# Kernel optimization log

Hardware: AMD Instinct MI355X
Metric: run time of the kernel (lower is better)

## Reference

```python
import jax, jax.numpy as jnp
import numpy as np

K_UPPER = 196608  # number of smallest-|grad| positions to mask per sample


def setup_inputs() -> dict:
    key = jax.random.key(0)
    k1, k2 = jax.random.split(key)
    x = jax.random.normal(k1, (64, 3, 512, 512), dtype=jnp.float32)
    grad = jax.random.normal(k2, (64, 3, 512, 512), dtype=jnp.float32)
    return {"x": x, "grad": grad}


def _mask_low_gradient(x, grad):
    # x, grad: [B, C, H, W]
    B, C, H, W = x.shape
    hw = H * W
    flat_g = grad.reshape(B, -1)                                  # [B, C*H*W]
    # _sort: k smallest absolute gradients -> top_k of negated abs (unsorted ok)
    _neg_vals, idx = jax.lax.top_k(-jnp.abs(flat_g), K_UPPER)     # idx: [B, K]
    # channel containing each selected flat index (matches the torch range test)
    ch = idx // hw                                                # [B, K]
    xc = x.reshape(B, C, hw)
    # Faithful to source: torch slice [start:channel_indexes] EXCLUDES the last
    # element of each channel when computing min/max.
    mn = jnp.min(xc[:, :, : hw - 1], axis=-1)                     # [B, C]
    mx = jnp.max(xc[:, :, : hw - 1], axis=-1)                     # [B, C]
    lo = jnp.take_along_axis(mn, ch, axis=1)                      # [B, K]
    hi = jnp.take_along_axis(mx, ch, axis=1)                      # [B, K]
    # uniform fill in [lo, hi) per masked element
    u = jax.random.uniform(jax.random.key(42), idx.shape, dtype=x.dtype)
    fill = lo + u * (hi - lo)                                     # [B, K]
    flat_x = x.reshape(B, -1)
    out = flat_x.at[jnp.arange(B)[:, None], idx].set(fill)
    return out.reshape(x.shape)


def reference(x, grad):
    return _mask_low_gradient(x, grad)
```

## Files before the change

kernel.cpp:

```cpp
#include <hip/hip_runtime.h>
#include <stdint.h>

#define TPB 256
#define TPS 1024

constexpr int BN   = 64;
constexpr int CCH  = 3;
constexpr int HWS  = 262144;
constexpr int LOG_HW = 18;
constexpr int NPS  = 786432;
constexpr int KSEL = 196608;
constexpr int KCAP = 200704;
constexpr int NB_T = 32;
constexpr int CH_T = NPS / NB_T;
constexpr int NB_C = 64;
constexpr int CH_C = NPS / NB_C;
constexpr int WCH  = CH_C / 4;
constexpr int NB_S = 8;
constexpr int CH_S = KCAP / NB_S;
constexpr int TILE = 4096;
constexpr int NBINS = 2048;
constexpr int SUB  = 8;
constexpr int NFB  = 49;
constexpr int ASLOT = 1024;
constexpr int ACAP = 256 * ASLOT;

typedef unsigned u32x4 __attribute__((ext_vector_type(4)));

constexpr int WS_MN   = 0;
constexpr int WS_MX   = 192;
constexpr int WS_V1   = 384;
constexpr int WS_B1   = 448;
constexpr int WS_V2   = 512;
constexpr int WS_GS   = 576;
constexpr int WS_KP   = 640;
constexpr int WS_S0   = 704;
constexpr int WS_S01  = 768;
constexpr int WS_CNT  = 832;
constexpr int WS_COFF = WS_CNT + BN * 256;
constexpr int WS_MNP  = WS_COFF + BN * 256;
constexpr int WS_MXP  = WS_MNP + BN * CCH * SUB;
constexpr int WS_CNT2 = WS_MXP + BN * CCH * SUB;
constexpr int WS_RC   = WS_CNT2 + BN * 256;
constexpr int WS_CHC  = WS_RC + BN * 256;
constexpr int WS_THA  = WS_CHC + BN * 4;
constexpr int WS_THB  = WS_THA + BN * NBINS;
constexpr int WS_H0   = WS_THB + BN * NBINS;
constexpr int WS_H1   = WS_H0 + BN * 256 * NB_S;
constexpr int WS_H2   = WS_H1 + BN * 256 * NB_S;
constexpr int WS_H3   = WS_H2 + BN * 256 * NB_S;
constexpr int WS_HF   = WS_H3 + BN * 256 * NB_S;
constexpr size_t WS_FIX_END = (size_t)WS_HF + (size_t)BN * 64 * NB_S;
constexpr size_t RECW = (size_t)BN * KCAP * 2;
constexpr size_t WS_NEEDED_BYTES = (WS_FIX_END + 2 * RECW) * 4;
static_assert((size_t)BN * ACAP <= RECW, "append scratch must fit in R2");

__device__ __forceinline__ unsigned rotl32(unsigned x, int r) { return (x << r) | (x >> (32 - r)); }

__device__ __forceinline__ void tf4(unsigned& x0, unsigned& x1, int a, int b, int c, int d) {
  x0 += x1; x1 = rotl32(x1, a); x1 ^= x0;
  x0 += x1; x1 = rotl32(x1, b); x1 ^= x0;
  x0 += x1; x1 = rotl32(x1, c); x1 ^= x0;
  x0 += x1; x1 = rotl32(x1, d); x1 ^= x0;
}

__device__ __forceinline__ void threefry2x32(unsigned k0, unsigned k1, unsigned c0, unsigned c1,
                                             unsigned& o0, unsigned& o1) {
  const unsigned ks2 = k0 ^ k1 ^ 0x1BD11BDAu;
  unsigned x0 = c0 + k0, x1 = c1 + k1;
  tf4(x0, x1, 13, 15, 26, 6);  x0 += k1;  x1 += ks2 + 1u;
  tf4(x0, x1, 17, 29, 16, 24); x0 += ks2; x1 += k0 + 2u;
  tf4(x0, x1, 13, 15, 26, 6);  x0 += k0;  x1 += k1 + 3u;
  tf4(x0, x1, 17, 29, 16, 24); x0 += k1;  x1 += ks2 + 4u;
  tf4(x0, x1, 13, 15, 26, 6);  x0 += ks2; x1 += k0 + 5u;
  o0 = x0; o1 = x1;
}

__global__ __launch_bounds__(TPB) void k_zero(unsigned* __restrict__ p, int n) {
  int i = blockIdx.x * TPB + threadIdx.x;
  if (i < n) p[i] = 0u;
}

__global__ __launch_bounds__(TPB) void k_mnmx(const float4* __restrict__ x,
                                              unsigned* __restrict__ ws) {
  __shared__ float smn[TPB], smx[TPB];
  const int g = blockIdx.x;
  const int bc = g / SUB, sub = g - bc * SUB;
  const int Q4 = HWS / 4 / SUB;
  const size_t base4 = (size_t)bc * (HWS / 4) + (size_t)sub * Q4;
  const bool last = (sub == SUB - 1);
  const int tid = threadIdx.x;
  float lo = 3.4e38f, hi = -3.4e38f;
  for (int i = tid; i < Q4; i += TPB) {
    float4 v = x[base4 + i];
    if (last && i == Q4 - 1) {
      lo = fminf(lo, fminf(fminf(v.x, v.y), v.z));
      hi = fmaxf(hi, fmaxf(fmaxf(v.x, v.y), v.z));
    } else {
      lo = fminf(lo, fminf(fminf(v.x, v.y), fminf(v.z, v.w)));
      hi = fmaxf(hi, fmaxf(fmaxf(v.x, v.y), fmaxf(v.z, v.w)));
    }
  }
  smn[tid] = lo; smx[tid] = hi; __syncthreads();
  for (int s = TPB / 2; s > 0; s >>= 1) {
    if (tid < s) { smn[tid] = fminf(smn[tid], smn[tid + s]); smx[tid] = fmaxf(smx[tid], smx[tid + s]); }
    __syncthreads();
  }
  if (tid == 0) {
    ((float*)(ws + WS_MNP))[g] = smn[0];
    ((float*)(ws + WS_MXP))[g] = smx[0];
  }
}

__global__ __launch_bounds__(TPB) void k_mnfin(unsigned* __restrict__ ws) {
  const int t = threadIdx.x;
  if (t < BN * CCH) {
    const float* mnp = (const float*)(ws + WS_MNP);
    const float* mxp = (const float*)(ws + WS_MXP);
    float lo = 3.4e38f, hi = -3.4e38f;
    for (int s = 0; s < SUB; ++s) {
      lo = fminf(lo, mnp[t * SUB + s]);
      hi = fmaxf(hi, mxp[t * SUB + s]);
    }
    ((float*)(ws + WS_MN))[t] = lo;
    ((float*)(ws + WS_MX))[t] = hi;
  }
}

__global__ __launch_bounds__(TPB) void k_thrA(const unsigned* __restrict__ gb, unsigned* __restrict__ hist) {
  __shared__ unsigned h[NBINS];
  const int b = blockIdx.y, blk = blockIdx.x, tid = threadIdx.x;
  for (int v = tid; v < NBINS; v += TPB) h[v] = 0u;
  __syncthreads();
  const uint4* g4 = (const uint4*)(gb + (size_t)b * NPS + (size_t)blk * CH_T);
  for (int i = tid; i < CH_T / 4; i += TPB) {
    uint4 v = g4[i];
    atomicAdd(&h[(v.x & 0x7FFFFFFFu) >> 21], 1u);
    atomicAdd(&h[(v.y & 0x7FFFFFFFu) >> 21], 1u);
    atomicAdd(&h[(v.z & 0x7FFFFFFFu) >> 21], 1u);
    atomicAdd(&h[(v.w & 0x7FFFFFFFu) >> 21], 1u);
  }
  __syncthreads();
  unsigned* gh = hist + (size_t)b * NBINS;
  for (int v = tid; v < NBINS; v += TPB) if (h[v]) atomicAdd(&gh[v], h[v]);
}

__global__ __launch_bounds__(TPB) void k_thrBC(const unsigned* __restrict__ gb,
                                               unsigned* __restrict__ hist,
                                               unsigned* __restrict__ app,
                                               unsigned* __restrict__ ws) {
  __shared__ unsigned h[NBINS];
  __shared__ unsigned chs[3];
  const int bid = blockIdx.x;
  const int b = bid & 63, blk = bid >> 6, tid = threadIdx.x;
  const int lane = tid & 63, wv = tid >> 6;
  const unsigned long long ltm = (1ull << lane) - 1ull;
  for (int v = tid; v < NBINS; v += TPB) h[v] = 0u;
  if (tid < 3) chs[tid] = 0u;
  __syncthreads();
  const unsigned V1 = ws[WS_V1 + b];
  const unsigned rangeId = (unsigned)(blk * 4 + wv);
  const uint4* g4 = (const uint4*)(gb + (size_t)b * NPS + (size_t)blk * CH_C) + wv * (WCH / 4);
  const unsigned e0 = (unsigned)blk * CH_C + (unsigned)wv * WCH;
  unsigned* ap = app + (size_t)b * ACAP + (size_t)rangeId * ASLOT;
  unsigned abase = 0;
  unsigned cntLess = 0, cc0 = 0, cc1 = 0, cc2 = 0;
  for (int it = 0; it < WCH / 256; ++it) {
    const uint4 v = g4[it * 64 + lane];
    const unsigned e = e0 + (unsigned)it * 256u + (unsigned)lane * 4u;
    const unsigned k[4] = { v.x & 0x7FFFFFFFu, v.y & 0x7FFFFFFFu, v.z & 0x7FFFFFFFu, v.w & 0x7FFFFFFFu };
#pragma unroll
    for (int c = 0; c < 4; ++c) {
      const unsigned top = k[c] >> 21;
      const bool isEq = (top == V1);
      if (top < V1) {
        ++cntLess;
        const unsigned ch = (e + (unsigned)c) >> LOG_HW;
        if (ch == 0) ++cc0; else if (ch == 1) ++cc1; else ++cc2;
      } else if (isEq) {
        atomicAdd(&h[(k[c] >> 10) & 2047u], 1u);
      }
      unsigned long long m = __ballot(isEq);
      if (isEq) {
        const unsigned ai = abase + (unsigned)__popcll(m & ltm);
        if (ai < (unsigned)ASLOT) {
          const unsigned ch = (e + (unsigned)c) >> LOG_HW;
          ap[ai] = (ch << 11) | ((k[c] >> 10) & 2047u);
        }
      }
      abase += (unsigned)__popcll(m);
    }
  }
  if (lane == 0) ws[WS_RC + b * 256 + rangeId] = min(abase, (unsigned)ASLOT);
  for (int off = 32; off >= 1; off >>= 1) cntLess += __shfl_down(cntLess, off, 64);
  if (lane == 0) ws[WS_CNT + b * 256 + rangeId] = cntLess;
  if (cc0) atomicAdd(&chs[0], cc0);
  if (cc1) atomicAdd(&chs[1], cc1);
  if (cc2) atomicAdd(&chs[2], cc2);
  __syncthreads();
  if (tid < 3 && chs[tid]) atomicAdd(&ws[WS_CHC + b * 4 + tid], chs[tid]);
  unsigned* gh = hist + (size_t)b * NBINS;
  for (int v = tid; v < NBINS; v += TPB) if (h[v]) atomicAdd(&gh[v], h[v]);
}

__global__ __launch_bounds__(TPB) void k_find(const unsigned* __restrict__ hist,
                                              unsigned* __restrict__ ws, int mode) {
  __shared__ unsigned part[TPB];
  const int b = blockIdx.x, tid = threadIdx.x;
  const unsigned* h = hist + (size_t)b * NBINS;
  const int per = NBINS / TPB;
  const unsigned Kt = (mode == 0) ? (unsigned)KSEL : (unsigned)KSEL - ws[WS_B1 + b];
  unsigned vals[8];
  unsigned s = 0;
  for (int j = 0; j < per; ++j) { vals[j] = h[tid * per + j]; s += vals[j]; }
  part[tid] = s; __syncthreads();
  for (int off = 1; off < TPB; off <<= 1) {
    unsigned t = (tid >= off) ? part[tid - off] : 0u;
    __syncthreads(); part[tid] += t; __syncthreads();
  }
  unsigned run = part[tid] - s;
  for (int j = 0; j < per; ++j) {
    const unsigned lo = run, c = vals[j];
    run += c;
    if (lo < Kt && Kt <= run) {
      const unsigned v = (unsigned)(tid * per + j);
      if (mode == 0) {
        ws[WS_V1 + b] = v; ws[WS_B1 + b] = lo;
      } else {
        ws[WS_V2 + b] = v;
        const unsigned T22 = (ws[WS_V1 + b] << 11) | v;
        ws[WS_GS + b] = (T22 << 10) | 1023u;
        unsigned kp = ws[WS_B1 + b] + lo + c;
        if (kp > (unsigned)KCAP) kp = (unsigned)KCAP;
        ws[WS_KP + b] = kp;
      }
    }
  }
}

__global__ __launch_bounds__(TPB) void k_cc2(const unsigned* __restrict__ app,
                                             unsigned* __restrict__ ws) {
  __shared__ unsigned lch[3];
  const int b = blockIdx.x, tid = threadIdx.x;
  if (tid < 3) lch[tid] = 0u;
  __syncthreads();
  const unsigned V2 = ws[WS_V2 + b];
  const unsigned cnt = ws[WS_RC + b * 256 + tid];
  const unsigned* ap = app + (size_t)b * ACAP + (size_t)tid * ASLOT;
  unsigned n2 = 0, c0 = 0, c1 = 0, c2 = 0;
  for (unsigned i = 0; i < cnt; ++i) {
    const unsigned e = ap[i];
    if ((e & 2047u) <= V2) {
      ++n2;
      const unsigned ch = (e >> 11) & 3u;
      if (ch == 0) ++c0; else if (ch == 1) ++c1; else ++c2;
    }
  }
  ws[WS_CNT2 + b * 256 + tid] = n2;
  if (c0) atomicAdd(&lch[0], c0);
  if (c1) atomicAdd(&lch[1], c1);
  if (c2) atomicAdd(&lch[2], c2);
  __syncthreads();
  if (tid < 3 && lch[tid]) atomicAdd(&ws[WS_CHC + b * 4 + tid], lch[tid]);
}

__global__ __launch_bounds__(TPB) void k_cscan(unsigned* __restrict__ ws) {
  __shared__ unsigned wsum[4];
  const int b = blockIdx.x, tid = threadIdx.x;
  const int lane = tid & 63, wv = tid >> 6;
  const unsigned cnt = ws[WS_CNT + b * 256 + tid] + ws[WS_CNT2 + b * 256 + tid];
  unsigned incl = cnt;
  for (int off = 1; off < 64; off <<= 1) {
    unsigned t = __shfl_up(incl, off, 64);
    if (lane >= off) incl += t;
  }
  if (lane == 63) wsum[wv] = incl;
  __syncthreads();
  unsigned wpre = 0;
  for (int w = 0; w < wv; ++w) wpre += wsum[w];
  ws[WS_COFF + b * 256 + tid] = incl - cnt + wpre;
  if (tid == 0) {
    const unsigned s0 = ws[WS_CHC + b * 4 + 0];
    ws[WS_S0 + b] = s0;
    ws[WS_S01 + b] = s0 + ws[WS_CHC + b * 4 + 1];
  }
}

__global__ __launch_bounds__(TPB) void k_cscatter(const unsigned* __restrict__ gb,
                                                  const unsigned* __restrict__ ws,
                                                  unsigned* __restrict__ keyArr,
                                                  unsigned* __restrict__ H0) {
  __shared__ unsigned h2[256 * NB_S];
  const int bid = blockIdx.x;
  const int b = bid & 63, blk = bid >> 6, tid = threadIdx.x;
  const int lane = tid & 63, wv = tid >> 6;
  for (int e = tid; e < 256 * NB_S; e += TPB) h2[e] = 0u;
  __syncthreads();
  const unsigned G = ws[WS_GS + b];
  unsigned base = ws[WS_COFF + b * 256 + blk * 4 + wv];
  const uint4* g4 = (const uint4*)(gb + (size_t)b * NPS + (size_t)blk * CH_C) + wv * (WCH / 4);
  unsigned* ka = keyArr + (size_t)b * KCAP;
  for (int it = 0; it < WCH / 256; ++it) {
    const uint4 v = g4[it * 64 + lane];
    unsigned k[4] = { v.x & 0x7FFFFFFFu, v.y & 0x7FFFFFFFu, v.z & 0x7FFFFFFFu, v.w & 0x7FFFFFFFu };
    bool s[4];
    unsigned cnt = 0;
#pragma unroll
    for (int c = 0; c < 4; ++c) { s[c] = (k[c] <= G); cnt += (unsigned)s[c]; }
    unsigned incl = cnt;
    for (int off = 1; off < 64; off <<= 1) {
      unsigned u = __shfl_up(incl, off, 64);
      if (lane >= off) incl += u;
    }
    const unsigned wtot = __shfl(incl, 63, 64);
    unsigned pos = base + incl - cnt;
#pragma unroll
    for (int c = 0; c < 4; ++c) {
      if (s[c]) {
        if (pos < (unsigned)KCAP) {
          ka[pos] = k[c];
          atomicAdd(&h2[(k[c] & 255u) * NB_S + pos / (unsigned)CH_S], 1u);
        }
        ++pos;
      }
    }
    base += wtot;
  }
  __syncthreads();
  unsigned* Hb = H0 + (size_t)b * 256 * NB_S;
  for (int e = tid; e < 256 * NB_S; e += TPB) {
    unsigned c = h2[e];
    if (c) atomicAdd(&Hb[e], c);
  }
}

__global__ __launch_bounds__(TPB) void k_hscan(unsigned* __restrict__ H) {
  __shared__ unsigned wsum[4];
  const int b = blockIdx.x, tid = threadIdx.x;
  const int lane = tid & 63, wv = tid >> 6;
  unsigned* Hb = H + (size_t)b * 256 * NB_S;
  unsigned row[NB_S];
  unsigned run = 0;
#pragma unroll
  for (int k = 0; k < NB_S; ++k) {
    unsigned t = Hb[tid * NB_S + k];
    row[k] = run; run += t;
  }
  unsigned incl = run;
  for (int off = 1; off < 64; off <<= 1) {
    unsigned t = __shfl_up(incl, off, 64);
    if (lane >= off) incl += t;
  }
  if (lane == 63) wsum[wv] = incl;
  __syncthreads();
  unsigned wpre = 0;
  for (int w = 0; w < wv; ++w) wpre += wsum[w];
  const unsigned excl = incl - run + wpre;
#pragma unroll
  for (int k = 0; k < NB_S; ++k) Hb[tid * NB_S + k] = row[k] + excl;
}

__global__ __launch_bounds__(64) void k_hscanF(unsigned* __restrict__ Hf) {
  const int b = blockIdx.x, tid = threadIdx.x;
  unsigned* Hb = Hf + (size_t)b * 64 * NB_S;
  unsigned row[NB_S];
  unsigned run = 0;
  if (tid < NFB) {
#pragma unroll
    for (int k = 0; k < NB_S; ++k) {
      unsigned t = Hb[tid * NB_S + k];
      row[k] = run; run += t;
    }
  }
  unsigned incl = run;
  for (int off = 1; off < 64; off <<= 1) {
    unsigned t = __shfl_up(incl, off, 64);
    if (tid >= off) incl += t;
  }
  const unsigned excl = incl - run;
  if (tid < NFB) {
#pragma unroll
    for (int k = 0; k < NB_S; ++k) Hb[tid * NB_S + k] = row[k] + excl;
  }
}

template<int MODE>
__global__ __launch_bounds__(TPS) void k_sort8(const unsigned* __restrict__ keyIn,
                                               const uint2* __restrict__ inR,
                                               uint2* __restrict__ outR,
                                               const unsigned* __restrict__ Hcur,
                                               unsigned* __restrict__ Hnext,
                                               unsigned* __restrict__ Hf,
                                               const unsigned* __restrict__ ws,
                                               int shift) {
  __shared__ unsigned wh[16][256];
  __shared__ unsigned gout[256];
  __shared__ unsigned gbase[256];
  __shared__ unsigned wsum[4];
  __shared__ uint2    stg[TILE];
  __shared__ unsigned h2[256 * NB_S];
  __shared__ unsigned h2f[(MODE == 1) ? NFB * NB_S : 1];
  const int bid = blockIdx.x;
  const int b = bid & 63, blk = bid >> 6, tid = threadIdx.x;
  const int lane = tid & 63, wv = tid >> 6;
  const unsigned long long ltm = (1ull << lane) - 1ull;
  const unsigned kp = min(ws[WS_KP + b], (unsigned)KCAP);
  const unsigned s0 = (unsigned)blk * CH_S;
  const unsigned s1 = min(s0 + (unsigned)CH_S, kp);
  const unsigned* ki = keyIn + (size_t)b * KCAP;
  const uint2* in = inR + (size_t)b * KCAP;
  uint2* out = outR + (size_t)b * KCAP;
  const bool doF = (MODE == 1) && (Hf != nullptr);

  for (int d = tid; d < 256; d += TPS) gbase[d] = Hcur[((size_t)b * 256 + d) * NB_S + blk];
  for (int e = tid; e < 256 * NB_S; e += TPS) h2[e] = 0u;
  if (MODE == 1) { if (doF) for (int e = tid; e < NFB * NB_S; e += TPS) h2f[e] = 0u; }
  __syncthreads();

  for (unsigned t0 = s0; t0 < s1; t0 += (unsigned)TILE) {
    { uint4* w4 = (uint4*)&wh[0][0];
      w4[tid] = make_uint4(0u, 0u, 0u, 0u); }
    __syncthreads();

    unsigned key[4], cpp[4], wloc[4], dig[4];
    bool val[4];
    const unsigned wbase = t0 + (unsigned)wv * 256u;
#pragma unroll
    for (int c = 0; c < 4; ++c) {
      const unsigned i = wbase + (unsigned)c * 64u + (unsigned)lane;
      val[c] = (i < s1);
      if (MODE == 0) { cpp[c] = i; key[c] = val[c] ? ki[i] : 0u; }
      else { uint2 r = val[c] ? in[i] : make_uint2(0u, 0u); cpp[c] = r.x; key[c] = r.y; }
      dig[c] = (key[c] >> shift) & 255u;
      unsigned long long peers = __ballot(val[c]);
#pragma unroll
      for (int bit = 0; bit < 8; ++bit) {
        unsigned long long bb = __ballot(val[c] && ((dig[c] >> bit) & 1u));
        peers &= ((dig[c] >> bit) & 1u) ? bb : ~bb;
      }
      const unsigned before = (unsigned)__popcll(peers & ltm);
      int ldr = __ffsll((unsigned long long)peers) - 1;
      if (ldr < 0) ldr = 0;
      unsigned old = 0;
      if (val[c] && lane == ldr) old = atomicAdd(&wh[wv][dig[c]], (unsigned)__popcll(peers));
      old = __shfl(old, ldr, 64);
      wloc[c] = old + before;
    }
    __syncthreads();

    unsigned incl = 0, tot = 0;
    if (tid < 256) {
      const unsigned d = (unsigned)tid;
#pragma unroll
      for (int w = 0; w < 16; ++w) tot += wh[w][d];
      incl = tot;
      for (int off = 1; off < 64; off <<= 1) {
        unsigned t = __shfl_up(incl, off, 64);
        if (lane >= off) incl += t;
      }
      if (lane == 63) wsum[wv] = incl;
    }
    __syncthreads();
    if (tid < 256) {
      const unsigned d = (unsigned)tid;
      unsigned wpre = 0;
      for (int w = 0; w < wv; ++w) wpre += wsum[w];
      const unsigned tstart = incl - tot + wpre;
      const unsigned g = gbase[d];
      gout[d] = g - tstart;
      gbase[d] = g + tot;
      unsigned run = tstart;
#pragma unroll
      for (int w = 0; w < 16; ++w) { const unsigned t = wh[w][d]; wh[w][d] = run; run += t; }
    }
    __syncthreads();

#pragma unroll
    for (int c = 0; c < 4; ++c) {
      if (val[c]) {
        uint2 r; r.x = cpp[c]; r.y = key[c];
        stg[wh[wv][dig[c]] + wloc[c]] = r;
      }
    }
    __syncthreads();
    const unsigned nt = min((unsigned)TILE, s1 - t0);
    for (unsigned j = tid; j < nt; j += TPS) {
      const uint2 r = stg[j];
      const unsigned d = (r.y >> shift) & 255u;
      const unsigned pos = gout[d] + j;
      out[pos] = r;
      const unsigned nd = (r.y >> (shift + 8)) & 255u;
      atomicAdd(&h2[nd * NB_S + pos / (unsigned)CH_S], 1u);
      if (doF) atomicAdd(&h2f[(r.x >> 12) * NB_S + pos / (unsigned)CH_S], 1u);
    }
    __syncthreads();
  }

  {
    unsigned* Hb = Hnext + (size_t)b * 256 * NB_S;
    for (int e = tid; e < 256 * NB_S; e += TPS) {
      unsigned c = h2[e];
      if (c) atomicAdd(&Hb[e], c);
    }
    if (doF) {
      unsigned* Hfb = Hf + (size_t)b * 64 * NB_S;
      for (int e = tid; e < NFB * NB_S; e += TPS) {
        unsigned c = h2f[e];
        if (c) atomicAdd(&Hfb[e], c);
      }
    }
  }
}

__global__ __launch_bounds__(TPS) void k_final(const uint2* __restrict__ inR,
                                               uint2* __restrict__ pairOut,
                                               const unsigned* __restrict__ Hcur,
                                               const unsigned* __restrict__ Hf,
                                               const unsigned* __restrict__ ws) {
  __shared__ unsigned wh[16][128];
  __shared__ unsigned gbase[128];
  __shared__ unsigned whF[16][64];
  __shared__ unsigned goutF[64];
  __shared__ unsigned gbaseF[64];
  __shared__ uint2    stg[TILE];
  const int bid = blockIdx.x;
  const int b = bid & 63, blk = bid >> 6, tid = threadIdx.x;
  const int lane = tid & 63, wv = tid >> 6;
  const unsigned long long ltm = (1ull << lane) - 1ull;
  const unsigned kp = min(ws[WS_KP + b], (unsigned)KCAP);
  const unsigned s0 = (unsigned)blk * CH_S;
  const unsigned s1 = min(s0 + (unsigned)CH_S, kp);
  const uint2* in = inR + (size_t)b * KCAP;
  uint2* po = pairOut + (size_t)b * KCAP;

  for (int d = tid; d < 128; d += TPS) gbase[d] = Hcur[((size_t)b * 256 + d) * NB_S + blk];
  for (int d = tid; d < 64; d += TPS)
    gbaseF[d] = (d < NFB) ? Hf[((size_t)b * 64 + d) * NB_S + blk] : 0u;
  __syncthreads();

  for (unsigned t0 = s0; t0 < s1; t0 += (unsigned)TILE) {
    { uint4* p = (uint4*)&wh[0][0];
      if (tid < 512) p[tid] = make_uint4(0u, 0u, 0u, 0u);
      uint4* q = (uint4*)&whF[0][0];
      if (tid >= 512 && tid < 768) q[tid - 512] = make_uint4(0u, 0u, 0u, 0u); }
    __syncthreads();

    unsigned key[4], cpp[4], wloc[4], dig[4];
    bool val[4];
    const unsigned wbase = t0 + (unsigned)wv * 256u;
#pragma unroll
    for (int c = 0; c < 4; ++c) {
      const unsigned i = wbase + (unsigned)c * 64u + (unsigned)lane;
      val[c] = (i < s1);
      uint2 r = val[c] ? in[i] : make_uint2(0u, 0u);
      cpp[c] = r.x; key[c] = r.y;
      dig[c] = (key[c] >> 24) & 127u;
      unsigned long long peers = __ballot(val[c]);
#pragma unroll
      for (int bit = 0; bit < 7; ++bit) {
        unsigned long long bb = __ballot(val[c] && ((dig[c] >> bit) & 1u));
        peers &= ((dig[c] >> bit) & 1u) ? bb : ~bb;
      }
      const unsigned before = (unsigned)__popcll(peers & ltm);
      int ldr = __ffsll((unsigned long long)peers) - 1;
      if (ldr < 0) ldr = 0;
      unsigned old = 0;
      if (val[c] && lane == ldr) old = atomicAdd(&wh[wv][dig[c]], (unsigned)__popcll(peers));
      old = __shfl(old, ldr, 64);
      wloc[c] = old + before;
    }
    __syncthreads();

    if (tid < 128) {
      const unsigned d = (unsigned)tid;
      unsigned run = gbase[d];
#pragma unroll
      for (int w = 0; w < 16; ++w) { const unsigned t = wh[w][d]; wh[w][d] = run; run += t; }
      gbase[d] = run;
    }
    __syncthreads();

    unsigned rnk[4], dbF[4], wlocF[4];
#pragma unroll
    for (int c = 0; c < 4; ++c) {
      dbF[c] = cpp[c] >> 12;
      if (val[c]) {
        rnk[c] = wh[wv][dig[c]] + wloc[c];
        wlocF[c] = atomicAdd(&whF[wv][dbF[c]], 1u);
      }
    }
    __syncthreads();

    if (tid < 64) {
      const unsigned d = (unsigned)tid;
      unsigned tot = 0;
      if (d < NFB) {
#pragma unroll
        for (int w = 0; w < 16; ++w) tot += whF[w][d];
      }
      unsigned incl = tot;
      for (int off = 1; off < 64; off <<= 1) {
        unsigned t = __shfl_up(incl, off, 64);
        if (lane >= off) incl += t;
      }
      const unsigned tstart = incl - tot;
      goutF[d] = gbaseF[d] - tstart;
      gbaseF[d] += tot;
      unsigned run = tstart;
#pragma unroll
      for (int w = 0; w < 16; ++w) { const unsigned t = whF[w][d]; whF[w][d] = run; run += t; }
    }
    __syncthreads();

#pragma unroll
    for (int c = 0; c < 4; ++c) {
      if (val[c]) {
        uint2 r; r.x = cpp[c]; r.y = rnk[c];
        stg[whF[wv][dbF[c]] + wlocF[c]] = r;
      }
    }
    __syncthreads();

    const unsigned nt = min((unsigned)TILE, s1 - t0);
    for (unsigned j = tid; j < nt; j += TPS) {
      const uint2 r = stg[j];
      po[goutF[r.x >> 12] + j] = r;
    }
    __syncthreads();
  }
}

__global__ __launch_bounds__(TPB) void k_unpack(const uint2* __restrict__ pairs,
                                                unsigned* __restrict__ fm,
                                                const unsigned* __restrict__ ws) {
  __shared__ unsigned vals[4096];
  const int bid = blockIdx.x;
  const int b = bid & 63, d = bid >> 6, tid = threadIdx.x;
  const unsigned kp = min(ws[WS_KP + b], (unsigned)KCAP);
  const unsigned start = (unsigned)d * 4096u;
  if (start >= kp) return;
  const unsigned cnt = min(4096u, kp - start);
  const unsigned S0 = ws[WS_S0 + b], S01 = ws[WS_S01 + b];
  const float* mnf = (const float*)(ws + WS_MN);
  const float* mxf = (const float*)(ws + WS_MX);
  const float l0 = mnf[b * CCH], l1 = mnf[b * CCH + 1], l2 = mnf[b * CCH + 2];
  const float h0 = mxf[b * CCH], h1 = mxf[b * CCH + 1], h2v = mxf[b * CCH + 2];
  const uint2* pb = pairs + (size_t)b * KCAP + start;
  for (unsigned j = tid; j < cnt; j += TPB) {
    const uint2 r = pb[j];
    unsigned res = 0xFFFFFFFFu;
    if (r.y < (unsigned)KSEL) {
      const unsigned p = (unsigned)b * (unsigned)KSEL + r.y;
      unsigned o0, o1;
      threefry2x32(0u, 42u, 0u, p, o0, o1);
      const unsigned bits = o0 ^ o1;
      const float u = __uint_as_float((bits >> 9) | 0x3f800000u) - 1.0f;
      const unsigned ch = (unsigned)(r.x >= S0) + (unsigned)(r.x >= S01);
      const float lo = (ch == 0) ? l0 : ((ch == 1) ? l1 : l2);
      const float hi = (ch == 0) ? h0 : ((ch == 1) ? h1 : h2v);
      res = __float_as_uint(lo + u * (hi - lo));
    }
    vals[r.x & 4095u] = res;
  }
  __syncthreads();
  unsigned* f = fm + (size_t)b * KCAP + start;
  for (unsigned j = tid; j < cnt; j += TPB) f[j] = vals[j];
}

__global__ __launch_bounds__(TPB) void k_fill(const u32x4* __restrict__ x4,
                                              const u32x4* __restrict__ g4all,
                                              const unsigned* __restrict__ fillmap,
                                              const unsigned* __restrict__ ws,
                                              u32x4* __restrict__ out4) {
  const int bid = blockIdx.x;
  const int b = bid & 63, blk = bid >> 6, tid = threadIdx.x;
  const int lane = tid & 63, wv = tid >> 6;
  const unsigned G = ws[WS_GS + b];
  const unsigned kp = min(ws[WS_KP + b], (unsigned)KCAP);
  unsigned base = ws[WS_COFF + b * 256 + blk * 4 + wv];
  const size_t t4 = (size_t)b * (NPS / 4) + (size_t)blk * (CH_C / 4) + (size_t)wv * (WCH / 4);
  const unsigned* fm = fillmap + (size_t)b * KCAP;
  for (int it = 0; it < WCH / 256; ++it) {
    const size_t a = t4 + it * 64 + lane;
    const u32x4 gv = __builtin_nontemporal_load(&g4all[a]);
    u32x4 xv = __builtin_nontemporal_load(&x4[a]);
    unsigned k[4] = { gv.x & 0x7FFFFFFFu, gv.y & 0x7FFFFFFFu, gv.z & 0x7FFFFFFFu, gv.w & 0x7FFFFFFFu };
    bool s[4];
    unsigned cnt = 0;
#pragma unroll
    for (int c = 0; c < 4; ++c) { s[c] = (k[c] <= G); cnt += (unsigned)s[c]; }
    unsigned incl = cnt;
    for (int off = 1; off < 64; off <<= 1) {
      unsigned u = __shfl_up(incl, off, 64);
      if (lane >= off) incl += u;
    }
    const unsigned wtot = __shfl(incl, 63, 64);
    unsigned pos = base + incl - cnt;
#pragma unroll
    for (int c = 0; c < 4; ++c) {
      if (s[c]) {
        if (pos < kp) {
          const unsigned r = fm[pos];
          if (r != 0xFFFFFFFFu) xv[c] = r;
        }
        ++pos;
      }
    }
    __builtin_nontemporal_store(xv, &out4[a]);
    base += wtot;
  }
}

extern "C" void kernel_launch(void* const* d_in, const int* in_sizes, int n_in,
                              void* d_out, int out_size, void* d_ws, size_t ws_size,
                              hipStream_t stream) {
  const float* x = (const float*)d_in[0];
  const unsigned* gb = (const unsigned*)d_in[1];
  float* out = (float*)d_out;
  unsigned* ws = (unsigned*)d_ws;
  if (ws_size < WS_NEEDED_BYTES) return;

  unsigned* R1 = ws + WS_FIX_END;
  unsigned* R2 = ws + WS_FIX_END + RECW;
  unsigned* H0 = ws + WS_H0;
  unsigned* H1 = ws + WS_H1;
  unsigned* H2 = ws + WS_H2;
  unsigned* H3 = ws + WS_H3;
  unsigned* HF = ws + WS_HF;

  dim3 blk(TPB);
  dim3 sblk(TPS);

  k_mnmx<<<dim3(BN * CCH * SUB), blk, 0, stream>>>((const float4*)x, ws);
  k_mnfin<<<dim3(1), blk, 0, stream>>>(ws);
  {
    const int nz = (int)(WS_FIX_END - WS_CHC);
    k_zero<<<dim3((nz + TPB - 1) / TPB), blk, 0, stream>>>(ws + WS_CHC, nz);
  }

  k_thrA<<<dim3(NB_T, BN), blk, 0, stream>>>(gb, ws + WS_THA);
  k_find<<<dim3(BN), blk, 0, stream>>>(ws + WS_THA, ws, 0);
  k_thrBC<<<dim3(NB_C * BN), blk, 0, stream>>>(gb, ws + WS_THB, R2, ws);
  k_find<<<dim3(BN), blk, 0, stream>>>(ws + WS_THB, ws, 1);
  k_cc2<<<dim3(BN), blk, 0, stream>>>(R2, ws);
  k_cscan<<<dim3(BN), blk, 0, stream>>>(ws);

  k_cscatter<<<dim3(NB_C * BN), blk, 0, stream>>>(gb, ws, R1, H0);

  k_hscan<<<dim3(BN), blk, 0, stream>>>(H0);
  k_sort8<0><<<dim3(NB_S * BN), sblk, 0, stream>>>(R1, (const uint2*)nullptr, (uint2*)R2, H0, H1, nullptr, ws, 0);
  k_hscan<<<dim3(BN), blk, 0, stream>>>(H1);
  k_sort8<1><<<dim3(NB_S * BN), sblk, 0, stream>>>(nullptr, (const uint2*)R2, (uint2*)R1, H1, H2, nullptr, ws, 8);
  k_hscan<<<dim3(BN), blk, 0, stream>>>(H2);
  k_sort8<1><<<dim3(NB_S * BN), sblk, 0, stream>>>(nullptr, (const uint2*)R1, (uint2*)R2, H2, H3, HF, ws, 16);
  k_hscan<<<dim3(BN), blk, 0, stream>>>(H3);
  k_hscanF<<<dim3(BN), dim3(64), 0, stream>>>(HF);

  k_final<<<dim3(NB_S * BN), sblk, 0, stream>>>((const uint2*)R2, (uint2*)R1, H3, HF, ws);
  k_unpack<<<dim3(NFB * BN), blk, 0, stream>>>((const uint2*)R1, R2, ws);

  k_fill<<<dim3(NB_C * BN), blk, 0, stream>>>((const u32x4*)x, (const u32x4*)gb, R2, ws, (u32x4*)out);
}
```

Baseline: 707.0 us.

## Write selection bitmap in scatter pass and read it in fill instead of grad

The compaction scatter kernel now packs the per-element selection predicate (|g| <= G) into a bitmap, one bit per element. The fill kernel reads this bitmap instead of re-reading the full gradient tensor, which cuts a large stream of global memory reads from the final pass. Ranges were also split three ways (768 per sample instead of 256) with smaller append slots, and the counting, scan and cc2 kernels were adapted to match. The bitmap path is used only when the workspace is large enough, otherwise the old path runs. The cost is extra bitmap writes and some shuffles in the scatter kernel.

```diff
diff --git a/kernel.cpp b/kernel.cpp
--- a/kernel.cpp
+++ b/kernel.cpp
@@ -15,15 +15,16 @@
 constexpr int CH_T = NPS / NB_T;
 constexpr int NB_C = 64;
 constexpr int CH_C = NPS / NB_C;
-constexpr int WCH  = CH_C / 4;
+constexpr int NRNG = 768;
 constexpr int NB_S = 8;
 constexpr int CH_S = KCAP / NB_S;
 constexpr int TILE = 4096;
 constexpr int NBINS = 2048;
 constexpr int SUB  = 8;
 constexpr int NFB  = 49;
-constexpr int ASLOT = 1024;
-constexpr int ACAP = 256 * ASLOT;
+constexpr int ASLOT = 256;
+constexpr int ACAP = NRNG * ASLOT;
+constexpr int BMPW = NPS / 32;
 
 typedef unsigned u32x4 __attribute__((ext_vector_type(4)));
 
@@ -37,12 +38,12 @@
 constexpr int WS_S0   = 704;
 constexpr int WS_S01  = 768;
 constexpr int WS_CNT  = 832;
-constexpr int WS_COFF = WS_CNT + BN * 256;
-constexpr int WS_MNP  = WS_COFF + BN * 256;
+constexpr int WS_COFF = WS_CNT + BN * NRNG;
+constexpr int WS_MNP  = WS_COFF + BN * NRNG;
 constexpr int WS_MXP  = WS_MNP + BN * CCH * SUB;
 constexpr int WS_CNT2 = WS_MXP + BN * CCH * SUB;
-constexpr int WS_RC   = WS_CNT2 + BN * 256;
-constexpr int WS_CHC  = WS_RC + BN * 256;
+constexpr int WS_RC   = WS_CNT2 + BN * NRNG;
+constexpr int WS_CHC  = WS_RC + BN * NRNG;
 constexpr int WS_THA  = WS_CHC + BN * 4;
 constexpr int WS_THB  = WS_THA + BN * NBINS;
 constexpr int WS_H0   = WS_THB + BN * NBINS;
@@ -53,6 +54,8 @@
 constexpr size_t WS_FIX_END = (size_t)WS_HF + (size_t)BN * 64 * NB_S;
 constexpr size_t RECW = (size_t)BN * KCAP * 2;
 constexpr size_t WS_NEEDED_BYTES = (WS_FIX_END + 2 * RECW) * 4;
+constexpr size_t WS_BMP_OFF = WS_FIX_END + 2 * RECW;
+constexpr size_t WS_NEEDED_BMP = (WS_BMP_OFF + (size_t)BN * BMPW) * 4;
 static_assert((size_t)BN * ACAP <= RECW, "append scratch must fit in R2");
 
 __device__ __forceinline__ unsigned rotl32(unsigned x, int r) { return (x << r) | (x >> (32 - r)); }
@@ -159,41 +162,47 @@
   if (tid < 3) chs[tid] = 0u;
   __syncthreads();
   const unsigned V1 = ws[WS_V1 + b];
-  const unsigned rangeId = (unsigned)(blk * 4 + wv);
-  const uint4* g4 = (const uint4*)(gb + (size_t)b * NPS + (size_t)blk * CH_C) + wv * (WCH / 4);
-  const unsigned e0 = (unsigned)blk * CH_C + (unsigned)wv * WCH;
-  unsigned* ap = app + (size_t)b * ACAP + (size_t)rangeId * ASLOT;
-  unsigned abase = 0;
-  unsigned cntLess = 0, cc0 = 0, cc1 = 0, cc2 = 0;
-  for (int it = 0; it < WCH / 256; ++it) {
-    const uint4 v = g4[it * 64 + lane];
-    const unsigned e = e0 + (unsigned)it * 256u + (unsigned)lane * 4u;
-    const unsigned k[4] = { v.x & 0x7FFFFFFFu, v.y & 0x7FFFFFFFu, v.z & 0x7FFFFFFFu, v.w & 0x7FFFFFFFu };
-#pragma unroll
-    for (int c = 0; c < 4; ++c) {
-      const unsigned top = k[c] >> 21;
-      const bool isEq = (top == V1);
-      if (top < V1) {
-        ++cntLess;
-        const unsigned ch = (e + (unsigned)c) >> LOG_HW;
-        if (ch == 0) ++cc0; else if (ch == 1) ++cc1; else ++cc2;
-      } else if (isEq) {
-        atomicAdd(&h[(k[c] >> 10) & 2047u], 1u);
-      }
-      unsigned long long m = __ballot(isEq);
-      if (isEq) {
-        const unsigned ai = abase + (unsigned)__popcll(m & ltm);
-        if (ai < (unsigned)ASLOT) {
+  const uint4* g4 = (const uint4*)(gb + (size_t)b * NPS + (size_t)blk * CH_C) + wv * 768;
+  unsigned cc0 = 0, cc1 = 0, cc2 = 0;
+  for (int r = 0; r < 3; ++r) {
+    const unsigned rangeId = (unsigned)((blk * 4 + wv) * 3 + r);
+    unsigned* ap = app + (size_t)b * ACAP + (size_t)rangeId * ASLOT;
+    unsigned abase = 0, cntLess = 0;
+#pragma unroll
+    for (int it = 0; it < 4; ++it) {
+      const uint4 v = g4[r * 256 + it * 64 + lane];
+      const unsigned e = (unsigned)blk * CH_C + (unsigned)wv * 3072u + (unsigned)r * 1024u
+                       + (unsigned)it * 256u + (unsigned)lane * 4u;
+      const unsigned k[4] = { v.x & 0x7FFFFFFFu, v.y & 0x7FFFFFFFu, v.z & 0x7FFFFFFFu, v.w & 0x7FFFFFFFu };
+#pragma unroll
+      for (int c = 0; c < 4; ++c) {
+        const unsigned top = k[c] >> 21;
+        const bool isEq = (top == V1);
+        if (top < V1) {
+          ++cntLess;
           const unsigned ch = (e + (unsigned)c) >> LOG_HW;
-          ap[ai] = (ch << 11) | ((k[c] >> 10) & 2047u);
+          if (ch == 0) ++cc0; else if (ch == 1) ++cc1; else ++cc2;
+        } else if (isEq) {
+          atomicAdd(&h[(k[c] >> 10) & 2047u], 1u);
         }
-      }
-      abase += (unsigned)__popcll(m);
-    }
-  }
-  if (lane == 0) ws[WS_RC + b * 256 + rangeId] = min(abase, (unsigned)ASLOT);
-  for (int off = 32; off >= 1; off >>= 1) cntLess += __shfl_down(cntLess, off, 64);
-  if (lane == 0) ws[WS_CNT + b * 256 + rangeId] = cntLess;
+        unsigned long long m = __ballot(isEq);
+        if (isEq) {
+          const unsigned ai = abase + (unsigned)__popcll(m & ltm);
+          if (ai < (unsigned)ASLOT) {
+            const unsigned ch = (e + (unsigned)c) >> LOG_HW;
+            ap[ai] = (ch << 11) | ((k[c] >> 10) & 2047u);
+          }
+        }
+        abase += (unsigned)__popcll(m);
+      }
+    }
+    unsigned cl = cntLess;
+    for (int off = 32; off >= 1; off >>= 1) cl += __shfl_down(cl, off, 64);
+    if (lane == 0) {
+      ws[WS_CNT + b * NRNG + rangeId] = cl;
+      ws[WS_RC + b * NRNG + rangeId] = min(abase, (unsigned)ASLOT);
+    }
+  }
   if (cc0) atomicAdd(&chs[0], cc0);
   if (cc1) atomicAdd(&chs[1], cc1);
   if (cc2) atomicAdd(&chs[2], cc2);
@@ -245,18 +254,22 @@
   if (tid < 3) lch[tid] = 0u;
   __syncthreads();
   const unsigned V2 = ws[WS_V2 + b];
-  const unsigned cnt = ws[WS_RC + b * 256 + tid];
-  const unsigned* ap = app + (size_t)b * ACAP + (size_t)tid * ASLOT;
-  unsigned n2 = 0, c0 = 0, c1 = 0, c2 = 0;
-  for (unsigned i = 0; i < cnt; ++i) {
-    const unsigned e = ap[i];
-    if ((e & 2047u) <= V2) {
-      ++n2;
-      const unsigned ch = (e >> 11) & 3u;
-      if (ch == 0) ++c0; else if (ch == 1) ++c1; else ++c2;
-    }
-  }
-  ws[WS_CNT2 + b * 256 + tid] = n2;
+  unsigned c0 = 0, c1 = 0, c2 = 0;
+  for (int j = 0; j < 3; ++j) {
+    const int r = j * 256 + tid;
+    const unsigned cnt = ws[WS_RC + b * NRNG + r];
+    const unsigned* ap = app + (size_t)b * ACAP + (size_t)r * ASLOT;
+    unsigned n2 = 0;
+    for (unsigned i = 0; i < cnt; ++i) {
+      const unsigned e = ap[i];
+      if ((e & 2047u) <= V2) {
+        ++n2;
+        const unsigned ch = (e >> 11) & 3u;
+        if (ch == 0) ++c0; else if (ch == 1) ++c1; else ++c2;
+      }
+    }
+    ws[WS_CNT2 + b * NRNG + r] = n2;
+  }
   if (c0) atomicAdd(&lch[0], c0);
   if (c1) atomicAdd(&lch[1], c1);
   if (c2) atomicAdd(&lch[2], c2);
@@ -268,8 +281,11 @@
   __shared__ unsigned wsum[4];
   const int b = blockIdx.x, tid = threadIdx.x;
   const int lane = tid & 63, wv = tid >> 6;
-  const unsigned cnt = ws[WS_CNT + b * 256 + tid] + ws[WS_CNT2 + b * 256 + tid];
-  unsigned incl = cnt;
+  const unsigned c0 = ws[WS_CNT + b * NRNG + 3 * tid + 0] + ws[WS_CNT2 + b * NRNG + 3 * tid + 0];
+  const unsigned c1 = ws[WS_CNT + b * NRNG + 3 * tid + 1] + ws[WS_CNT2 + b * NRNG + 3 * tid + 1];
+  const unsigned c2 = ws[WS_CNT + b * NRNG + 3 * tid + 2] + ws[WS_CNT2 + b * NRNG + 3 * tid + 2];
+  const unsigned s = c0 + c1 + c2;
+  unsigned incl = s;
   for (int off = 1; off < 64; off <<= 1) {
     unsigned t = __shfl_up(incl, off, 64);
     if (lane >= off) incl += t;
@@ -278,7 +294,10 @@
   __syncthreads();
   unsigned wpre = 0;
   for (int w = 0; w < wv; ++w) wpre += wsum[w];
-  ws[WS_COFF + b * 256 + tid] = incl - cnt + wpre;
+  const unsigned excl = incl - s + wpre;
+  ws[WS_COFF + b * NRNG + 3 * tid + 0] = excl;
+  ws[WS_COFF + b * NRNG + 3 * tid + 1] = excl + c0;
+  ws[WS_COFF + b * NRNG + 3 * tid + 2] = excl + c0 + c1;
   if (tid == 0) {
     const unsigned s0 = ws[WS_CHC + b * 4 + 0];
     ws[WS_S0 + b] = s0;
@@ -286,10 +305,12 @@
   }
 }
 
+template<int BMP>
 __global__ __launch_bounds__(TPB) void k_cscatter(const unsigned* __restrict__ gb,
                                                   const unsigned* __restrict__ ws,
                                                   unsigned* __restrict__ keyArr,
-                                                  unsigned* __restrict__ H0) {
+                                                  unsigned* __restrict__ H0,
+                                                  unsigned* __restrict__ bmp) {
   __shared__ unsigned h2[256 * NB_S];
   const int bid = blockIdx.x;
   const int b = bid & 63, blk = bid >> 6, tid = threadIdx.x;
@@ -297,34 +318,50 @@
   for (int e = tid; e < 256 * NB_S; e += TPB) h2[e] = 0u;
   __syncthreads();
   const unsigned G = ws[WS_GS + b];
-  unsigned base = ws[WS_COFF + b * 256 + blk * 4 + wv];
-  const uint4* g4 = (const uint4*)(gb + (size_t)b * NPS + (size_t)blk * CH_C) + wv * (WCH / 4);
+  const uint4* g4 = (const uint4*)(gb + (size_t)b * NPS + (size_t)blk * CH_C) + wv * 768;
   unsigned* ka = keyArr + (size_t)b * KCAP;
-  for (int it = 0; it < WCH / 256; ++it) {
-    const uint4 v = g4[it * 64 + lane];
-    unsigned k[4] = { v.x & 0x7FFFFFFFu, v.y & 0x7FFFFFFFu, v.z & 0x7FFFFFFFu, v.w & 0x7FFFFFFFu };
-    bool s[4];
-    unsigned cnt = 0;
-#pragma unroll
-    for (int c = 0; c < 4; ++c) { s[c] = (k[c] <= G); cnt += (unsigned)s[c]; }
-    unsigned incl = cnt;
-    for (int off = 1; off < 64; off <<= 1) {
-      unsigned u = __shfl_up(incl, off, 64);
-      if (lane >= off) incl += u;
-    }
-    const unsigned wtot = __shfl(incl, 63, 64);
-    unsigned pos = base + incl - cnt;
-#pragma unroll
-    for (int c = 0; c < 4; ++c) {
-      if (s[c]) {
-        if (pos < (unsigned)KCAP) {
-          ka[pos] = k[c];
-          atomicAdd(&h2[(k[c] & 255u) * NB_S + pos / (unsigned)CH_S], 1u);
+  unsigned* bw = BMP ? (bmp + (size_t)b * BMPW + (size_t)blk * 384 + (size_t)wv * 96) : nullptr;
+  for (int r = 0; r < 3; ++r) {
+    unsigned base = ws[WS_COFF + b * NRNG + (blk * 4 + wv) * 3 + r];
+#pragma unroll
+    for (int it = 0; it < 4; ++it) {
+      const uint4 v = g4[r * 256 + it * 64 + lane];
+      unsigned k[4] = { v.x & 0x7FFFFFFFu, v.y & 0x7FFFFFFFu, v.z & 0x7FFFFFFFu, v.w & 0x7FFFFFFFu };
+      unsigned nib = 0;
+      unsigned cnt = 0;
+      bool s[4];
+#pragma unroll
+      for (int c = 0; c < 4; ++c) {
+        s[c] = (k[c] <= G);
+        nib |= ((unsigned)s[c]) << c;
+        cnt += (unsigned)s[c];
+      }
+      if (BMP) {
+        unsigned w = nib << ((lane & 7) * 4);
+        w |= __shfl_xor(w, 1, 64);
+        w |= __shfl_xor(w, 2, 64);
+        w |= __shfl_xor(w, 4, 64);
+        if ((lane & 7) == 0) bw[r * 32 + it * 8 + (lane >> 3)] = w;
+      }
+      unsigned incl = cnt;
+      for (int off = 1; off < 64; off <<= 1) {
+        unsigned u = __shfl_up(incl, off, 64);
+        if (lane >= off) incl += u;
+      }
+      const unsigned wtot = __shfl(incl, 63, 64);
+      unsigned pos = base + incl - cnt;
+#pragma unroll
+      for (int c = 0; c < 4; ++c) {
+        if (s[c]) {
+          if (pos < (unsigned)KCAP) {
+            ka[pos] = k[c];
+            atomicAdd(&h2[(k[c] & 255u) * NB_S + pos / (unsigned)CH_S], 1u);
+          }
+          ++pos;
         }
-        ++pos;
-      }
-    }
-    base += wtot;
+      }
+      base += wtot;
+    }
   }
   __syncthreads();
   unsigned* Hb = H0 + (size_t)b * 256 * NB_S;
@@ -667,8 +704,10 @@
   for (unsigned j = tid; j < cnt; j += TPB) f[j] = vals[j];
 }
 
+template<int BMP>
 __global__ __launch_bounds__(TPB) void k_fill(const u32x4* __restrict__ x4,
                                               const u32x4* __restrict__ g4all,
+                                              const unsigned* __restrict__ bmp,
                                               const unsigned* __restrict__ fillmap,
                                               const unsigned* __restrict__ ws,
                                               u32x4* __restrict__ out4) {
@@ -677,37 +716,47 @@
   const int lane = tid & 63, wv = tid >> 6;
   const unsigned G = ws[WS_GS + b];
   const unsigned kp = min(ws[WS_KP + b], (unsigned)KCAP);
-  unsigned base = ws[WS_COFF + b * 256 + blk * 4 + wv];
-  const size_t t4 = (size_t)b * (NPS / 4) + (size_t)blk * (CH_C / 4) + (size_t)wv * (WCH / 4);
+  const size_t t4 = (size_t)b * (NPS / 4) + (size_t)blk * (CH_C / 4) + (size_t)wv * 768;
   const unsigned* fm = fillmap + (size_t)b * KCAP;
-  for (int it = 0; it < WCH / 256; ++it) {
-    const size_t a = t4 + it * 64 + lane;
-    const u32x4 gv = __builtin_nontemporal_load(&g4all[a]);
-    u32x4 xv = __builtin_nontemporal_load(&x4[a]);
-    unsigned k[4] = { gv.x & 0x7FFFFFFFu, gv.y & 0x7FFFFFFFu, gv.z & 0x7FFFFFFFu, gv.w & 0x7FFFFFFFu };
-    bool s[4];
-    unsigned cnt = 0;
-#pragma unroll
-    for (int c = 0; c < 4; ++c) { s[c] = (k[c] <= G); cnt += (unsigned)s[c]; }
-    unsigned incl = cnt;
-    for (int off = 1; off < 64; off <<= 1) {
-      unsigned u = __shfl_up(incl, off, 64);
-      if (lane >= off) incl += u;
-    }
-    const unsigned wtot = __shfl(incl, 63, 64);
-    unsigned pos = base + incl - cnt;
-#pragma unroll
-    for (int c = 0; c < 4; ++c) {
-      if (s[c]) {
-        if (pos < kp) {
-          const unsigned r = fm[pos];
-          if (r != 0xFFFFFFFFu) xv[c] = r;
+  const unsigned* bw = BMP ? (bmp + (size_t)b * BMPW + (size_t)blk * 384 + (size_t)wv * 96) : nullptr;
+  for (int r = 0; r < 3; ++r) {
+    unsigned base = ws[WS_COFF + b * NRNG + (blk * 4 + wv) * 3 + r];
+#pragma unroll
+    for (int it = 0; it < 4; ++it) {
+      const size_t a = t4 + r * 256 + it * 64 + lane;
+      u32x4 xv = __builtin_nontemporal_load(&x4[a]);
+      unsigned nib;
+      if (BMP) {
+        const unsigned w = bw[r * 32 + it * 8 + (lane >> 3)];
+        nib = (w >> ((lane & 7) * 4)) & 0xFu;
+      } else {
+        const u32x4 gv = __builtin_nontemporal_load(&g4all[a]);
+        nib = (unsigned)((gv.x & 0x7FFFFFFFu) <= G)
+            | ((unsigned)((gv.y & 0x7FFFFFFFu) <= G) << 1)
+            | ((unsigned)((gv.z & 0x7FFFFFFFu) <= G) << 2)
+            | ((unsigned)((gv.w & 0x7FFFFFFFu) <= G) << 3);
+      }
+      const unsigned cnt = (unsigned)__popc(nib);
+      unsigned incl = cnt;
+      for (int off = 1; off < 64; off <<= 1) {
+        unsigned u = __shfl_up(incl, off, 64);
+        if (lane >= off) incl += u;
+      }
+      const unsigned wtot = __shfl(incl, 63, 64);
+      unsigned pos = base + incl - cnt;
+#pragma unroll
+      for (int c = 0; c < 4; ++c) {
+        if ((nib >> c) & 1u) {
+          if (pos < kp) {
+            const unsigned rr = fm[pos];
+            if (rr != 0xFFFFFFFFu) xv[c] = rr;
+          }
+          ++pos;
         }
-        ++pos;
-      }
-    }
-    __builtin_nontemporal_store(xv, &out4[a]);
-    base += wtot;
+      }
+      __builtin_nontemporal_store(xv, &out4[a]);
+      base += wtot;
+    }
   }
 }
 
@@ -719,9 +768,11 @@
   float* out = (float*)d_out;
   unsigned* ws = (unsigned*)d_ws;
   if (ws_size < WS_NEEDED_BYTES) return;
+  const bool useBmp = (ws_size >= WS_NEEDED_BMP);
 
   unsigned* R1 = ws + WS_FIX_END;
   unsigned* R2 = ws + WS_FIX_END + RECW;
+  unsigned* BMP = ws + WS_BMP_OFF;
   unsigned* H0 = ws + WS_H0;
   unsigned* H1 = ws + WS_H1;
   unsigned* H2 = ws + WS_H2;
@@ -745,7 +796,8 @@
   k_cc2<<<dim3(BN), blk, 0, stream>>>(R2, ws);
   k_cscan<<<dim3(BN), blk, 0, stream>>>(ws);
 
-  k_cscatter<<<dim3(NB_C * BN), blk, 0, stream>>>(gb, ws, R1, H0);
+  if (useBmp) k_cscatter<1><<<dim3(NB_C * BN), blk, 0, stream>>>(gb, ws, R1, H0, BMP);
+  else        k_cscatter<0><<<dim3(NB_C * BN), blk, 0, stream>>>(gb, ws, R1, H0, nullptr);
 
   k_hscan<<<dim3(BN), blk, 0, stream>>>(H0);
   k_sort8<0><<<dim3(NB_S * BN), sblk, 0, stream>>>(R1, (const uint2*)nullptr, (uint2*)R2, H0, H1, nullptr, ws, 0);
@@ -759,5 +811,6 @@
   k_final<<<dim3(NB_S * BN), sblk, 0, stream>>>((const uint2*)R2, (uint2*)R1, H3, HF, ws);
   k_unpack<<<dim3(NFB * BN), blk, 0, stream>>>((const uint2*)R1, R2, ws);
 
-  k_fill<<<dim3(NB_C * BN), blk, 0, stream>>>((const u32x4*)x, (const u32x4*)gb, R2, ws, (u32x4*)out);
-}
+  if (useBmp) k_fill<1><<<dim3(NB_C * BN), blk, 0, stream>>>((const u32x4*)x, nullptr, BMP, R2, ws, (u32x4*)out);
+  else        k_fill<0><<<dim3(NB_C * BN), blk, 0, stream>>>((const u32x4*)x, (const u32x4*)gb, nullptr, R2, ws, (u32x4*)out);
+}
```

Measured after the change: 708.5 us, median of 2. About the same (+0.2%).
